# Performance work log

Measured on AMD Instinct MI355X. Metric: run time of the kernel, lower is better.

## Reference

```python
import jax, jax.numpy as jnp
import numpy as np

V, D, L, H, HD, S = 50257, 768, 8, 6, 128, 2048
BS = 128          # flex-attention BLOCK_SIZE
EOS = 50256       # document separator token
EPS = 1.1920929e-07  # torch F.rms_norm default eps (f32 machine eps)
ATTN_SCALE = 0.12


def rms(x):
    return x * jax.lax.rsqrt(jnp.mean(jnp.square(x), axis=-1, keepdims=True) + EPS)


def rope_tables(seq_len, hd):
    # modded-nanogpt rotary: hd//4 geometric freqs + hd//4 zero freqs, applied to half-split dims
    freqs = (1.0 / 1024.0) ** jnp.linspace(0.0, 1.0, hd // 4)
    freqs = jnp.concatenate([freqs, jnp.zeros(hd // 4, dtype=jnp.float32)])
    theta = jnp.arange(seq_len, dtype=jnp.float32)[:, None] * freqs[None, :]  # [S, hd//2]
    return jnp.cos(theta), jnp.sin(theta)


def rope(x, cos, sin):  # x: [B,S,H,hd]
    x1, x2 = jnp.split(x, 2, axis=-1)
    c = cos[None, :, None, :]
    s = sin[None, :, None, :]
    return jnp.concatenate([x1 * c + x2 * s, -x1 * s + x2 * c], axis=-1)


def build_token_mask(input_seq, w):
    # Reproduces BlockMask.from_kv_blocks semantics: per query-row keep the w-1 most
    # recent FULL blocks and min(n_partial, max(w - n_full, 1)) most recent PARTIAL
    # blocks; mask_mod (document-causal) applies inside partial blocks only.
    NB = S // BS
    docs = jnp.cumsum((input_seq == EOS).astype(jnp.int32))
    bi = jnp.arange(NB)
    dr = docs.reshape(NB, BS)
    dl, dh = dr[:, 0], dr[:, -1]
    m_any = (bi[:, None] >= bi[None, :]) & (dl[:, None] <= dh[None, :]) & (dh[:, None] >= dl[None, :])
    m_all = (bi[:, None] > bi[None, :]) & (dl[:, None] == dh[None, :]) & (dh[:, None] == dl[None, :])
    part = m_any & ~m_all
    nf = m_all.sum(-1)

    def keep_most_recent(m, kcount):  # keep kcount True entries with largest kv index
        r = jnp.cumsum(m[:, ::-1].astype(jnp.int32), axis=-1)[:, ::-1]
        return m & (r <= kcount[:, None])

    kf = keep_most_recent(m_all, jnp.minimum(nf, w - 1))
    kp = keep_most_recent(part, jnp.minimum(part.sum(-1), jnp.maximum(w - nf, 1)))
    tf = jnp.repeat(jnp.repeat(kf, BS, 0), BS, 1)   # [S,S]
    tp = jnp.repeat(jnp.repeat(kp, BS, 0), BS, 1)
    q = jnp.arange(S)
    tok = (q[:, None] >= q[None, :]) & (docs[:, None] == docs[None, :])
    return tf | (tp & tok)


def _forward(input_seq, sliding_window_num_blocks, target_seq, embed, ve_embeds,
             qkv_w, attn_proj_w, mlp_fc_w, mlp_proj_w, scalars):
    cos, sin = rope_tables(S, HD)
    long_m = build_token_mask(input_seq, sliding_window_num_blocks)
    short_m = build_token_mask(input_seq, sliding_window_num_blocks // 2)
    cycle = [long_m, short_m, short_m, short_m]
    masks = (cycle * ((L + 3) // 4))[:L - 1] + [long_m]

    ve_tok = ve_embeds[:, input_seq, :]  # [3,S,D]
    ve = [ve_tok[0], ve_tok[1], ve_tok[2]] + [None] * (L - 6) + [ve_tok[0], ve_tok[1], ve_tok[2]]

    skip_w = scalars[:L]
    lambdas = scalars[L:3 * L].reshape(L, 2)
    sa_lambdas = scalars[3 * L:5 * L].reshape(L, 2)

    stride = max(1, L // 4)
    skip_map = {}
    for m in range(3):
        i = L - 3 + m
        j = i - stride * (m + 1)
        if 0 <= j < i < L:
            skip_map[i] = j

    x = x0 = rms(embed[input_seq])[None]  # [1,S,D]
    skips = []
    for i in range(L):
        if i in skip_map:
            x = x + skip_w[skip_map[i]] * skips[skip_map[i]]
        lam, sal = lambdas[i], sa_lambdas[i]
        # Block: residual mix with x0, attn, mlp (modded-nanogpt style)
        x = lam[0] * x + lam[1] * x0
        xa = rms(x)
        qkv = (xa @ qkv_w[i].T).reshape(1, S, 3 * H, HD)
        q, k, v = jnp.split(qkv, 3, axis=2)
        q = rope(rms(q), cos, sin)
        k = rope(rms(k), cos, sin)
        if ve[i] is not None:
            v = sal[0] * v + sal[1] * ve[i].reshape(1, S, H, HD)
        else:
            v = sal[0] * v
        scores = jnp.einsum('bqhd,bkhd->bhqk', q, k) * ATTN_SCALE
        scores = jnp.where(masks[i][None, None], scores, -jnp.inf)
        y = jnp.einsum('bhqk,bkhd->bqhd', jax.nn.softmax(scores, axis=-1), v)
        x = x + y.reshape(1, S, H * HD) @ attn_proj_w[i].T
        h = jnp.square(jax.nn.relu(rms(x) @ mlp_fc_w[i].T))
        x = x + h @ mlp_proj_w[i].T
        skips.append(x)

    x = rms(x)
    logits = (x[0].astype(jnp.bfloat16) @ embed.T.astype(jnp.bfloat16)).astype(jnp.float32)
    cap = 15.0 * logits * jax.lax.rsqrt(jnp.square(logits) + 225.0)  # softcap
    lsm = jax.nn.log_softmax(cap, axis=-1)
    return -jnp.mean(lsm[jnp.arange(S), target_seq])


def setup_inputs() -> dict:
    key = jax.random.key(0)
    ks = jax.random.split(key, 9)
    input_seq = jax.random.randint(ks[0], (S,), 0, V)
    input_seq = input_seq.at[jnp.arange(0, S, 512)].set(EOS)  # inject doc boundaries
    target_seq = jax.random.randint(ks[1], (S,), 0, V)
    embed = jax.random.normal(ks[2], (V, D), jnp.float32)
    ve_embeds = jax.random.normal(ks[3], (3, V, D), jnp.float32)
    sd = 1.0 / np.sqrt(D)
    qkv_w = jax.random.normal(ks[4], (L, 3 * H * HD, D), jnp.float32) * sd
    attn_proj_w = jax.random.normal(ks[5], (L, D, H * HD), jnp.float32) * (1.0 / np.sqrt(H * HD))
    mlp_fc_w = jax.random.normal(ks[6], (L, 4 * D, D), jnp.float32) * sd
    mlp_proj_w = jax.random.normal(ks[7], (L, D, 4 * D), jnp.float32) * (1.0 / np.sqrt(4 * D))
    scalars = jnp.concatenate([
        jnp.ones(L), jnp.tile(jnp.array([1.0, 0.0]), L), jnp.tile(jnp.array([0.5, 0.5]), L)
    ]).astype(jnp.float32) + 0.02 * jax.random.normal(ks[8], (5 * L,), jnp.float32)
    return {"input_seq": input_seq, "sliding_window_num_blocks": 8, "target_seq": target_seq,
            "embed": embed, "ve_embeds": ve_embeds, "qkv_w": qkv_w, "attn_proj_w": attn_proj_w,
            "mlp_fc_w": mlp_fc_w, "mlp_proj_w": mlp_proj_w, "scalars": scalars}


def reference(input_seq, sliding_window_num_blocks, target_seq, embed, ve_embeds,
              qkv_w, attn_proj_w, mlp_fc_w, mlp_proj_w, scalars):
    return _forward(input_seq, sliding_window_num_blocks, target_seq, embed, ve_embeds,
                    qkv_w, attn_proj_w, mlp_fc_w, mlp_proj_w, scalars)
```

## Files before the change

kernel.cpp:

```cpp
#include <hip/hip_runtime.h>
#include <hip/hip_bf16.h>
#include <math.h>

#define NSEQ 2048
#define NDIM 768
#define NLAY 8
#define NHEAD 6
#define NHD 128
#define NVOC 50257
#define NBLK 16
#define BLKSZ 128
#define EOS_TOK 50256
#define EPSF 1.1920929e-07f
#define ASCALE 0.12f
#define NVT 393
#define CAPSH 15.f

#define GSWZ(r) (((r) ^ ((r) >> 2)) & 3)

using bf16x8 = __attribute__((ext_vector_type(8))) __bf16;
using bf16x4 = __attribute__((ext_vector_type(4))) __bf16;
using f32x4  = __attribute__((ext_vector_type(4))) float;

__device__ __forceinline__ __bf16 tobf(float x) {
  __hip_bfloat16 h = __float2bfloat16(x);
  return *reinterpret_cast<__bf16*>(&h);
}

__global__ __launch_bounds__(256) void cvt_bf16_kernel(const float* __restrict__ in, __bf16* __restrict__ out,
                                                       long n) {
  long i = ((long)blockIdx.x * blockDim.x + threadIdx.x) * 4;
  long stride = (long)gridDim.x * blockDim.x * 4;
  for (; i < n; i += stride) {
    float4 v = *(const float4*)(in + i);
    bf16x4 o;
    o[0] = tobf(v.x); o[1] = tobf(v.y); o[2] = tobf(v.z); o[3] = tobf(v.w);
    *(bf16x4*)(out + i) = o;
  }
}

__global__ __launch_bounds__(1024) void prep_kernel(const int* __restrict__ seq, const int* __restrict__ wptr,
                                                    int* __restrict__ docs, int* __restrict__ catL,
                                                    int* __restrict__ catS) {
  __shared__ int f[NSEQ];
  __shared__ int g[NSEQ];
  int tid = threadIdx.x;
  for (int i = tid; i < NSEQ; i += 1024) f[i] = (seq[i] == EOS_TOK) ? 1 : 0;
  __syncthreads();
  int* a = f; int* b = g;
  for (int off = 1; off < NSEQ; off <<= 1) {
    for (int i = tid; i < NSEQ; i += 1024) {
      int v = a[i];
      if (i >= off) v += a[i - off];
      b[i] = v;
    }
    __syncthreads();
    int* t = a; a = b; b = t;
  }
  for (int i = tid; i < NSEQ; i += 1024) docs[i] = a[i];
  __syncthreads();
  if (tid == 0) {
    int dl[NBLK], dh[NBLK];
    for (int bi = 0; bi < NBLK; ++bi) { dl[bi] = a[bi * BLKSZ]; dh[bi] = a[bi * BLKSZ + BLKSZ - 1]; }
    int W = *wptr;
    for (int pass = 0; pass < 2; ++pass) {
      int w = (pass == 0) ? W : (W / 2);
      int* cat = (pass == 0) ? catL : catS;
      for (int i = 0; i < NBLK; ++i) {
        int allr[NBLK], partr[NBLK];
        int nf = 0, np = 0;
        for (int j = 0; j < NBLK; ++j) {
          int any_ = (i >= j) && (dl[i] <= dh[j]) && (dh[i] >= dl[j]);
          int all_ = (i > j) && (dl[i] == dh[j]) && (dh[i] == dl[j]);
          allr[j] = all_; partr[j] = any_ && !all_;
          nf += all_; np += partr[j];
        }
        int kcf = min(nf, w - 1);
        int kcp = min(np, max(w - nf, 1));
        int cf = 0, cp = 0;
        for (int j = NBLK - 1; j >= 0; --j) {
          int cv = 0;
          if (allr[j]) { cf++; if (cf <= kcf) cv = 2; }
          if (partr[j]) { cp++; if (cp <= kcp) cv = 1; }
          cat[i * NBLK + j] = cv;
        }
      }
    }
  }
}

__global__ __launch_bounds__(256) void embed_rms_kernel(const int* __restrict__ seq, const float* __restrict__ embed,
                                                        float* __restrict__ x, float* __restrict__ x0) {
  int s = blockIdx.x;
  int tid = threadIdx.x;
  const float* row = embed + (size_t)seq[s] * NDIM;
  float v0 = row[tid], v1 = row[tid + 256], v2 = row[tid + 512];
  float ss = v0 * v0 + v1 * v1 + v2 * v2;
  __shared__ float red[256];
  red[tid] = ss; __syncthreads();
  for (int o = 128; o > 0; o >>= 1) { if (tid < o) red[tid] += red[tid + o]; __syncthreads(); }
  float sc = rsqrtf(red[0] / (float)NDIM + EPSF);
  size_t base = (size_t)s * NDIM;
  float o0 = v0 * sc, o1 = v1 * sc, o2 = v2 * sc;
  x[base + tid] = o0; x[base + tid + 256] = o1; x[base + tid + 512] = o2;
  x0[base + tid] = o0; x0[base + tid + 256] = o1; x0[base + tid + 512] = o2;
}

__global__ __launch_bounds__(256) void rmsbf_kernel(const float* __restrict__ x, __bf16* __restrict__ xb) {
  int s = blockIdx.x;
  int tid = threadIdx.x;
  size_t base = (size_t)s * NDIM;
  float v0 = x[base + tid], v1 = x[base + tid + 256], v2 = x[base + tid + 512];
  float ss = v0 * v0 + v1 * v1 + v2 * v2;
  __shared__ float red[256];
  red[tid] = ss; __syncthreads();
  for (int o = 128; o > 0; o >>= 1) { if (tid < o) red[tid] += red[tid + o]; __syncthreads(); }
  float sc = rsqrtf(red[0] / (float)NDIM + EPSF);
  xb[base + tid] = tobf(v0 * sc); xb[base + tid + 256] = tobf(v1 * sc); xb[base + tid + 512] = tobf(v2 * sc);
}

__global__ __launch_bounds__(256) void mixrms_kernel(float* __restrict__ x, const float* __restrict__ x0,
                                                     const float* __restrict__ skip, const float* __restrict__ scal,
                                                     int li, int sj, __bf16* __restrict__ xb) {
  float lam0 = scal[NLAY + 2 * li], lam1 = scal[NLAY + 2 * li + 1];
  float sw = (sj >= 0) ? scal[sj] : 0.f;
  int s = blockIdx.x;
  int tid = threadIdx.x;
  size_t base = (size_t)s * NDIM;
  float xv[3], ov[3], nv[3];
  xv[0] = x[base + tid]; xv[1] = x[base + tid + 256]; xv[2] = x[base + tid + 512];
  ov[0] = x0[base + tid]; ov[1] = x0[base + tid + 256]; ov[2] = x0[base + tid + 512];
  if (skip) {
    nv[0] = lam0 * (xv[0] + sw * skip[base + tid])       + lam1 * ov[0];
    nv[1] = lam0 * (xv[1] + sw * skip[base + tid + 256]) + lam1 * ov[1];
    nv[2] = lam0 * (xv[2] + sw * skip[base + tid + 512]) + lam1 * ov[2];
  } else {
    nv[0] = lam0 * xv[0] + lam1 * ov[0];
    nv[1] = lam0 * xv[1] + lam1 * ov[1];
    nv[2] = lam0 * xv[2] + lam1 * ov[2];
  }
  x[base + tid] = nv[0]; x[base + tid + 256] = nv[1]; x[base + tid + 512] = nv[2];
  float ss = nv[0] * nv[0] + nv[1] * nv[1] + nv[2] * nv[2];
  __shared__ float red[256];
  red[tid] = ss; __syncthreads();
  for (int o = 128; o > 0; o >>= 1) { if (tid < o) red[tid] += red[tid + o]; __syncthreads(); }
  float sc = rsqrtf(red[0] / (float)NDIM + EPSF);
  xb[base + tid] = tobf(nv[0] * sc); xb[base + tid + 256] = tobf(nv[1] * sc); xb[base + tid + 512] = tobf(nv[2] * sc);
}

template <int MODE>
__global__ __launch_bounds__(256) void gemm_mfma(const __bf16* __restrict__ A, const __bf16* __restrict__ B,
                                                 float* __restrict__ Cf, __bf16* __restrict__ Cb,
                                                 int N, int K) {
  __shared__ __bf16 As[2][128 * 32];
  __shared__ __bf16 Bs[2][128 * 32];
  int bm = blockIdx.x * 128, bn = blockIdx.y * 128;
  int tid = threadIdx.x;
  int w = tid >> 6, l = tid & 63;
  int wm = (w >> 1) * 64, wn = (w & 1) * 64;
  int c = l & 15, g = l >> 4;

  auto stage = [&](int buf, int k0) {
#pragma unroll
    for (int i = 0; i < 2; ++i) {
      int L = (w * 2 + i) * 64 + l;
      int row = L >> 2, gc = L & 3;
      int gs = gc ^ GSWZ(row);
      const __bf16* srcA = A + (size_t)(bm + row) * K + k0 + gs * 8;
      const __bf16* srcB = B + (size_t)(bn + row) * K + k0 + gs * 8;
      __builtin_amdgcn_global_load_lds(
          (const __attribute__((address_space(1))) void*)srcA,
          (__attribute__((address_space(3))) void*)&As[buf][(w * 2 + i) * 512], 16, 0, 0);
      __builtin_amdgcn_global_load_lds(
          (const __attribute__((address_space(1))) void*)srcB,
          (__attribute__((address_space(3))) void*)&Bs[buf][(w * 2 + i) * 512], 16, 0, 0);
    }
  };

  f32x4 acc[4][4] = {};
  stage(0, 0);
  __syncthreads();
  int nk = K >> 5;
  for (int kk = 0; kk < nk; ++kk) {
    int buf = kk & 1;
    if (kk + 1 < nk) stage(buf ^ 1, (kk + 1) * 32);
    bf16x8 af[4], bfr[4];
#pragma unroll
    for (int i = 0; i < 4; ++i) {
      int row = wm + i * 16 + c;
      af[i] = *(const bf16x8*)&As[buf][row * 32 + (g ^ GSWZ(row)) * 8];
    }
#pragma unroll
    for (int j = 0; j < 4; ++j) {
      int row = wn + j * 16 + c;
      bfr[j] = *(const bf16x8*)&Bs[buf][row * 32 + (g ^ GSWZ(row)) * 8];
    }
#pragma unroll
    for (int i = 0; i < 4; ++i)
#pragma unroll
      for (int j = 0; j < 4; ++j)
        acc[i][j] = __builtin_amdgcn_mfma_f32_16x16x32_bf16(af[i], bfr[j], acc[i][j], 0, 0, 0);
    __syncthreads();
  }
#pragma unroll
  for (int i = 0; i < 4; ++i)
#pragma unroll
    for (int j = 0; j < 4; ++j)
#pragma unroll
      for (int rr = 0; rr < 4; ++rr) {
        int row = bm + wm + i * 16 + g * 4 + rr;
        int col = bn + wn + j * 16 + c;
        size_t ci = (size_t)row * N + col;
        float z = acc[i][j][rr];
        if (MODE == 0) Cf[ci] = z;
        else if (MODE == 1) Cf[ci] += z;
        else { float r = fmaxf(z, 0.f); Cb[ci] = tobf(r * r); }
      }
}

template <int MODE>
__global__ __launch_bounds__(256) void gemm_mfma64(const __bf16* __restrict__ A, const __bf16* __restrict__ B,
                                                   float* __restrict__ Cf, __bf16* __restrict__ Cb,
                                                   int N, int K) {
  __shared__ __bf16 As[2][64 * 32];
  __shared__ __bf16 Bs[2][64 * 32];
  int bm = blockIdx.x * 64, bn = blockIdx.y * 64;
  int tid = threadIdx.x;
  int w = tid >> 6, l = tid & 63;
  int wm = (w >> 1) * 32, wn = (w & 1) * 32;
  int c = l & 15, g = l >> 4;

  auto stage = [&](int buf, int k0) {
    int L = w * 64 + l;
    int row = L >> 2, gc = L & 3;
    int gs = gc ^ GSWZ(row);
    const __bf16* srcA = A + (size_t)(bm + row) * K + k0 + gs * 8;
    const __bf16* srcB = B + (size_t)(bn + row) * K + k0 + gs * 8;
    __builtin_amdgcn_global_load_lds(
        (const __attribute__((address_space(1))) void*)srcA,
        (__attribute__((address_space(3))) void*)&As[buf][w * 512], 16, 0, 0);
    __builtin_amdgcn_global_load_lds(
        (const __attribute__((address_space(1))) void*)srcB,
        (__attribute__((address_space(3))) void*)&Bs[buf][w * 512], 16, 0, 0);
  };

  f32x4 acc[2][2] = {};
  stage(0, 0);
  __syncthreads();
  int nk = K >> 5;
  for (int kk = 0; kk < nk; ++kk) {
    int buf = kk & 1;
    if (kk + 1 < nk) stage(buf ^ 1, (kk + 1) * 32);
    bf16x8 af[2], bfr[2];
#pragma unroll
    for (int i = 0; i < 2; ++i) {
      int row = wm + i * 16 + c;
      af[i] = *(const bf16x8*)&As[buf][row * 32 + (g ^ GSWZ(row)) * 8];
    }
#pragma unroll
    for (int j = 0; j < 2; ++j) {
      int row = wn + j * 16 + c;
      bfr[j] = *(const bf16x8*)&Bs[buf][row * 32 + (g ^ GSWZ(row)) * 8];
    }
#pragma unroll
    for (int i = 0; i < 2; ++i)
#pragma unroll
      for (int j = 0; j < 2; ++j)
        acc[i][j] = __builtin_amdgcn_mfma_f32_16x16x32_bf16(af[i], bfr[j], acc[i][j], 0, 0, 0);
    __syncthreads();
  }
#pragma unroll
  for (int i = 0; i < 2; ++i)
#pragma unroll
    for (int j = 0; j < 2; ++j)
#pragma unroll
      for (int rr = 0; rr < 4; ++rr) {
        int row = bm + wm + i * 16 + g * 4 + rr;
        int col = bn + wn + j * 16 + c;
        size_t ci = (size_t)row * N + col;
        float z = acc[i][j][rr];
        if (MODE == 0) Cf[ci] = z;
        else if (MODE == 1) Cf[ci] += z;
        else { float r = fmaxf(z, 0.f); Cb[ci] = tobf(r * r); }
      }
}

__global__ __launch_bounds__(256) void qkv_post_kernel(const float* __restrict__ qkv, const float* __restrict__ vemb,
                                                       const int* __restrict__ seq, const float* __restrict__ scal,
                                                       int li, int ve_idx,
                                                       __bf16* __restrict__ qo, __bf16* __restrict__ ko,
                                                       __bf16* __restrict__ vo) {
  int p = blockIdx.x * 4 + (threadIdx.x >> 6);
  int l = threadIdx.x & 63;
  int h = p >> 11;
  int s = p & (NSEQ - 1);
  float sal0 = scal[3 * NLAY + 2 * li], sal1 = scal[3 * NLAY + 2 * li + 1];
  float fr = (l < 32) ? powf(1.0f / 1024.0f, (float)l * (1.0f / 31.0f)) : 0.f;
  float th = (float)s * fr;
  float cth = cosf(th), sth = sinf(th);
  size_t rb = (size_t)s * (3 * NHEAD * NHD) + h * NHD;
  float q0 = qkv[rb + l],                 q1 = qkv[rb + l + 64];
  float k0 = qkv[rb + NHEAD * NHD + l],   k1 = qkv[rb + NHEAD * NHD + l + 64];
  float v0 = qkv[rb + 2 * NHEAD * NHD + l], v1 = qkv[rb + 2 * NHEAD * NHD + l + 64];
  float ssq = q0 * q0 + q1 * q1;
  float ssk = k0 * k0 + k1 * k1;
#pragma unroll
  for (int o = 1; o < 64; o <<= 1) {
    ssq += __shfl_xor(ssq, o, 64);
    ssk += __shfl_xor(ssk, o, 64);
  }
  float scq = rsqrtf(ssq / (float)NHD + EPSF);
  float sck = rsqrtf(ssk / (float)NHD + EPSF);
  float qn0 = q0 * scq, qn1 = q1 * scq;
  float kn0 = k0 * sck, kn1 = k1 * sck;
  float oq0 = qn0 * cth + qn1 * sth, oq1 = -qn0 * sth + qn1 * cth;
  float ok0 = kn0 * cth + kn1 * sth, ok1 = -kn0 * sth + kn1 * cth;
  float ov0 = sal0 * v0, ov1 = sal0 * v1;
  if (ve_idx >= 0) {
    const float* ver = vemb + ((size_t)ve_idx * NVOC + seq[s]) * NDIM + h * NHD;
    ov0 += sal1 * ver[l];
    ov1 += sal1 * ver[l + 64];
  }
  size_t oo = ((size_t)h * NSEQ + s) * NHD;
  qo[oo + l] = tobf(oq0); qo[oo + l + 64] = tobf(oq1);
  ko[oo + l] = tobf(ok0); ko[oo + l + 64] = tobf(ok1);
  vo[oo + l] = tobf(ov0); vo[oo + l + 64] = tobf(ov1);
}

__global__ __launch_bounds__(256) void vtrans_kernel(const __bf16* __restrict__ v, __bf16* __restrict__ vt) {
  int st = blockIdx.x * 64, dt = blockIdx.y * 64, h = blockIdx.z;
  __shared__ __bf16 t[64][65];
  int tid = threadIdx.x;
  for (int e = tid; e < 4096; e += 256) {
    int s = e >> 6, d = e & 63;
    t[s][d] = v[((size_t)h * NSEQ + st + s) * NHD + dt + d];
  }
  __syncthreads();
  for (int e = tid; e < 512; e += 256) {
    int d = e >> 3, s0 = (e & 7) * 8;
    bf16x8 ov;
#pragma unroll
    for (int i = 0; i < 8; ++i) ov[i] = t[s0 + i][d];
    *(bf16x8*)(vt + ((size_t)h * NHD + dt + d) * NSEQ + st + s0) = ov;
  }
}

__global__ __launch_bounds__(128) void attn_mfma_kernel(const __bf16* __restrict__ qb, const __bf16* __restrict__ kb,
                                                        const __bf16* __restrict__ vt, const int* __restrict__ cat,
                                                        const int* __restrict__ docs, __bf16* __restrict__ y) {
  int qb32 = (int)gridDim.x - 1 - (int)blockIdx.x;
  int h = blockIdx.y;
  int tid = threadIdx.x;
  int wq = tid >> 6;
  int l = tid & 63;
  int c = l & 15, g = l >> 4;
  int q0 = qb32 * 32 + wq * 16;
  int qB = qb32 >> 2;

  __shared__ __bf16 Ks[2][32 * 128];
  __shared__ __bf16 Vts[2][32 * 128];
  __shared__ __bf16 Ps[2][16 * 32];
  __shared__ int kvs[64];
  __shared__ int kvc[64];
  __shared__ int nact_s;

  if (tid == 0) {
    int n = 0;
    for (int kv = 0; kv <= qb32; ++kv) {
      int cc = cat[qB * NBLK + (kv >> 2)];
      if (cc) { kvs[n] = kv; kvc[n] = cc; ++n; }
    }
    nact_s = n;
  }

  bf16x8 qf[4];
#pragma unroll
  for (int ks = 0; ks < 4; ++ks)
    qf[ks] = *(const bf16x8*)(qb + ((size_t)h * NSEQ + q0 + c) * NHD + ks * 32 + g * 8);

  int qd[4];
#pragma unroll
  for (int rr = 0; rr < 4; ++rr) qd[rr] = docs[q0 + g * 4 + rr];

  float m[4], lden[4];
#pragma unroll
  for (int rr = 0; rr < 4; ++rr) { m[rr] = -INFINITY; lden[rr] = 0.f; }
  f32x4 oacc[8] = {};

  __syncthreads();
  int nact = nact_s;

  auto stage = [&](int kv, int bufi) {
#pragma unroll
    for (int i = 0; i < 4; ++i) {
      int L = (wq * 4 + i) * 64 + l;
      int krow = L >> 4, gl = L & 15;
      int gs = gl ^ (krow & 7);
      const __bf16* srcK = kb + ((size_t)h * NSEQ + kv * 32 + krow) * NHD + gs * 8;
      __builtin_amdgcn_global_load_lds(
          (const __attribute__((address_space(1))) void*)srcK,
          (__attribute__((address_space(3))) void*)&Ks[bufi][(wq * 4 + i) * 512], 16, 0, 0);
      int drow = L >> 2, gk = L & 3;
      const __bf16* srcV = vt + ((size_t)h * NHD + drow) * NSEQ + kv * 32 + gk * 8;
      __builtin_amdgcn_global_load_lds(
          (const __attribute__((address_space(1))) void*)srcV,
          (__attribute__((address_space(3))) void*)&Vts[bufi][(wq * 4 + i) * 512], 16, 0, 0);
    }
  };

  stage(kvs[0], 0);
  __syncthreads();

  for (int it = 0; it < nact; ++it) {
    int buf = it & 1;
    if (it + 1 < nact) stage(kvs[it + 1], buf ^ 1);
    int kv = kvs[it], cc = kvc[it];
    int k0 = kv * 32;

    f32x4 sacc[2] = {};
#pragma unroll
    for (int ks = 0; ks < 4; ++ks) {
#pragma unroll
      for (int j = 0; j < 2; ++j) {
        int row = j * 16 + c;
        int gi = (ks * 4 + g) ^ (row & 7);
        bf16x8 kf = *(const bf16x8*)&Ks[buf][row * 128 + gi * 8];
        sacc[j] = __builtin_amdgcn_mfma_f32_16x16x32_bf16(qf[ks], kf, sacc[j], 0, 0, 0);
      }
    }
    float sc[2][4];
    float bmax[4] = {-INFINITY, -INFINITY, -INFINITY, -INFINITY};
#pragma unroll
    for (int j = 0; j < 2; ++j) {
      int key = k0 + j * 16 + c;
      int kdj = docs[key];
#pragma unroll
      for (int rr = 0; rr < 4; ++rr) {
        int qrow = q0 + g * 4 + rr;
        bool ok = (cc == 2) || ((key <= qrow) && (kdj == qd[rr]));
        float z = ok ? sacc[j][rr] * ASCALE : -INFINITY;
        sc[j][rr] = z;
        bmax[rr] = fmaxf(bmax[rr], z);
      }
    }
#pragma unroll
    for (int rr = 0; rr < 4; ++rr) {
      bmax[rr] = fmaxf(bmax[rr], __shfl_xor(bmax[rr], 1, 64));
      bmax[rr] = fmaxf(bmax[rr], __shfl_xor(bmax[rr], 2, 64));
      bmax[rr] = fmaxf(bmax[rr], __shfl_xor(bmax[rr], 4, 64));
      bmax[rr] = fmaxf(bmax[rr], __shfl_xor(bmax[rr], 8, 64));
    }
    float corr[4], psum[4];
#pragma unroll
    for (int rr = 0; rr < 4; ++rr) {
      float mnew = fmaxf(m[rr], bmax[rr]);
      float msafe = (mnew == -INFINITY) ? 0.f : mnew;
      corr[rr] = __expf(m[rr] - msafe);
      float p0 = __expf(sc[0][rr] - msafe);
      float p1 = __expf(sc[1][rr] - msafe);
      sc[0][rr] = p0; sc[1][rr] = p1;
      psum[rr] = p0 + p1;
      m[rr] = mnew;
    }
#pragma unroll
    for (int rr = 0; rr < 4; ++rr) {
      psum[rr] += __shfl_xor(psum[rr], 1, 64);
      psum[rr] += __shfl_xor(psum[rr], 2, 64);
      psum[rr] += __shfl_xor(psum[rr], 4, 64);
      psum[rr] += __shfl_xor(psum[rr], 8, 64);
      lden[rr] = lden[rr] * corr[rr] + psum[rr];
    }
#pragma unroll
    for (int nt = 0; nt < 8; ++nt)
#pragma unroll
      for (int rr = 0; rr < 4; ++rr) oacc[nt][rr] *= corr[rr];
#pragma unroll
    for (int j = 0; j < 2; ++j)
#pragma unroll
      for (int rr = 0; rr < 4; ++rr)
        Ps[wq][(g * 4 + rr) * 32 + j * 16 + c] = tobf(sc[j][rr]);
    asm volatile("s_waitcnt lgkmcnt(0)" ::: "memory");
    bf16x8 pf = *(const bf16x8*)&Ps[wq][c * 32 + g * 8];
#pragma unroll
    for (int nt = 0; nt < 8; ++nt) {
      bf16x8 vf = *(const bf16x8*)&Vts[buf][(nt * 16 + c) * 32 + g * 8];
      oacc[nt] = __builtin_amdgcn_mfma_f32_16x16x32_bf16(pf, vf, oacc[nt], 0, 0, 0);
    }
    __syncthreads();
  }
  float inv[4];
#pragma unroll
  for (int rr = 0; rr < 4; ++rr) inv[rr] = (lden[rr] > 0.f) ? 1.f / lden[rr] : 0.f;
#pragma unroll
  for (int nt = 0; nt < 8; ++nt)
#pragma unroll
    for (int rr = 0; rr < 4; ++rr) {
      int qrow = q0 + g * 4 + rr;
      y[(size_t)qrow * NDIM + h * NHD + nt * 16 + c] = tobf(oacc[nt][rr] * inv[rr]);
    }
}

__global__ __launch_bounds__(256) void logits_gemm_kernel(const __bf16* __restrict__ xbf,
                                                          const __bf16* __restrict__ embed_bf,
                                                          const int* __restrict__ target,
                                                          float* __restrict__ part_l,
                                                          float* __restrict__ tcap) {
  __shared__ __bf16 As[2][128 * 32];
  __shared__ __bf16 Bs[2][128 * 32];
  __shared__ float rs2[2][128];
  int lid = (int)blockIdx.y * (int)gridDim.x + (int)blockIdx.x;
  int nid = (lid & 7) * 786 + (lid >> 3);
  int bm = (nid & 15) * 128;
  int vt = nid >> 4;
  int bn = vt * 128;
  int tid = threadIdx.x;
  int w = tid >> 6, l = tid & 63;
  int wm = (w >> 1) * 64, wn = (w & 1) * 64;
  int c = l & 15, g = l >> 4;

  auto stage = [&](int buf, int k0) {
#pragma unroll
    for (int i = 0; i < 2; ++i) {
      int L = (w * 2 + i) * 64 + l;
      int row = L >> 2, gc = L & 3;
      int gs = gc ^ GSWZ(row);
      int vrow = bn + row;
      if (vrow >= NVOC) vrow = NVOC - 1;
      const __bf16* srcA = xbf + (size_t)(bm + row) * NDIM + k0 + gs * 8;
      const __bf16* srcB = embed_bf + (size_t)vrow * NDIM + k0 + gs * 8;
      __builtin_amdgcn_global_load_lds(
          (const __attribute__((address_space(1))) void*)srcA,
          (__attribute__((address_space(3))) void*)&As[buf][(w * 2 + i) * 512], 16, 0, 0);
      __builtin_amdgcn_global_load_lds(
          (const __attribute__((address_space(1))) void*)srcB,
          (__attribute__((address_space(3))) void*)&Bs[buf][(w * 2 + i) * 512], 16, 0, 0);
    }
  };

  f32x4 acc[4][4] = {};
  stage(0, 0);
  __syncthreads();
  const int nk = NDIM / 32;
  for (int kk = 0; kk < nk; ++kk) {
    int buf = kk & 1;
    if (kk + 1 < nk) stage(buf ^ 1, (kk + 1) * 32);
    bf16x8 af[4], bfr[4];
#pragma unroll
    for (int i = 0; i < 4; ++i) {
      int row = wm + i * 16 + c;
      af[i] = *(const bf16x8*)&As[buf][row * 32 + (g ^ GSWZ(row)) * 8];
    }
#pragma unroll
    for (int j = 0; j < 4; ++j) {
      int row = wn + j * 16 + c;
      bfr[j] = *(const bf16x8*)&Bs[buf][row * 32 + (g ^ GSWZ(row)) * 8];
    }
#pragma unroll
    for (int i = 0; i < 4; ++i)
#pragma unroll
      for (int j = 0; j < 4; ++j)
        acc[i][j] = __builtin_amdgcn_mfma_f32_16x16x32_bf16(af[i], bfr[j], acc[i][j], 0, 0, 0);
    __syncthreads();
  }

#pragma unroll
  for (int i = 0; i < 4; ++i) {
#pragma unroll
    for (int rr = 0; rr < 4; ++rr) {
      int rowl = wm + i * 16 + g * 4 + rr;
      int tg = target[bm + rowl];
      float ts = 0.f;
#pragma unroll
      for (int j = 0; j < 4; ++j) {
        int vv = bn + wn + j * 16 + c;
        bool okv = vv < NVOC;
        float z = acc[i][j][rr];
        float cp = 15.f * z * rsqrtf(z * z + 225.f);
        ts += okv ? __expf(cp - CAPSH) : 0.f;
        if (okv && vv == tg) tcap[bm + rowl] = cp;
      }
      ts += __shfl_xor(ts, 1, 64);
      ts += __shfl_xor(ts, 2, 64);
      ts += __shfl_xor(ts, 4, 64);
      ts += __shfl_xor(ts, 8, 64);
      if (c == 0) rs2[w & 1][rowl] = ts;
    }
  }
  __syncthreads();
  if (tid < 128) {
    part_l[(size_t)vt * NSEQ + bm + tid] = rs2[0][tid] + rs2[1][tid];
  }
}

__global__ __launch_bounds__(256) void lossrow_kernel(const float* __restrict__ part_l,
                                                      const float* __restrict__ tcap, float* __restrict__ lr) {
  int row = blockIdx.x * 256 + threadIdx.x;
  float L = 0.f;
  for (int cc = 0; cc < NVT; ++cc) L += part_l[(size_t)cc * NSEQ + row];
  lr[row] = (CAPSH + logf(L)) - tcap[row];
}

__global__ __launch_bounds__(256) void loss2_kernel(const float* __restrict__ lr, float* __restrict__ out) {
  int tid = threadIdx.x;
  float sum = 0.f;
  for (int t = tid; t < NSEQ; t += 256) sum += lr[t];
  __shared__ float red[256];
  red[tid] = sum; __syncthreads();
  for (int o = 128; o > 0; o >>= 1) { if (tid < o) red[tid] += red[tid + o]; __syncthreads(); }
  if (tid == 0) out[0] = red[0] / (float)NSEQ;
}

extern "C" void kernel_launch(void* const* d_in, const int* in_sizes, int n_in,
                              void* d_out, int out_size, void* d_ws, size_t ws_size,
                              hipStream_t stream) {
  const int* seq   = (const int*)d_in[0];
  const int* wnb   = (const int*)d_in[1];
  const int* tgt   = (const int*)d_in[2];
  const float* embed = (const float*)d_in[3];
  const float* vemb  = (const float*)d_in[4];
  const float* qkvw  = (const float*)d_in[5];
  const float* aprj  = (const float*)d_in[6];
  const float* fcw   = (const float*)d_in[7];
  const float* prjw  = (const float*)d_in[8];
  const float* scal  = (const float*)d_in[9];
  float* out = (float*)d_out;

  char* w = (char*)d_ws;
  auto alloc = [&](size_t bytes) {
    char* p = w;
    w += (bytes + 255) & ~(size_t)255;
    return p;
  };
  int* docs = (int*)alloc(NSEQ * 4);
  int* catL = (int*)alloc(NBLK * NBLK * 4);
  int* catS = (int*)alloc(NBLK * NBLK * 4);
  float* x    = (float*)alloc((size_t)NSEQ * NDIM * 4);
  float* x0   = (float*)alloc((size_t)NSEQ * NDIM * 4);
  float* sk1  = (float*)alloc((size_t)NSEQ * NDIM * 4);
  float* sk2  = (float*)alloc((size_t)NSEQ * NDIM * 4);
  float* sk3  = (float*)alloc((size_t)NSEQ * NDIM * 4);
  float* qkvb = (float*)alloc((size_t)NSEQ * 3 * NHEAD * NHD * 4);
  __bf16* qbf2 = (__bf16*)alloc((size_t)NHEAD * NSEQ * NHD * 2);
  __bf16* kbf2 = (__bf16*)alloc((size_t)NHEAD * NSEQ * NHD * 2);
  __bf16* vbf2 = (__bf16*)alloc((size_t)NHEAD * NSEQ * NHD * 2);
  __bf16* vtbf = (__bf16*)alloc((size_t)NHEAD * NHD * NSEQ * 2);
  __bf16* xabf = (__bf16*)alloc((size_t)NSEQ * NDIM * 2);
  __bf16* ybf  = (__bf16*)alloc((size_t)NSEQ * NDIM * 2);
  __bf16* hbf  = (__bf16*)alloc((size_t)NSEQ * 4 * NDIM * 2);
  __bf16* xbf  = (__bf16*)alloc((size_t)NSEQ * NDIM * 2);
  float* pl   = (float*)alloc((size_t)NVT * NSEQ * 4);
  float* tc   = (float*)alloc((size_t)NSEQ * 4);
  float* lrow = (float*)alloc((size_t)NSEQ * 4);
  __bf16* embbf = (__bf16*)alloc((size_t)NVOC * NDIM * 2);
  __bf16* qkvwbf = (__bf16*)alloc((size_t)NLAY * 3 * NHEAD * NHD * NDIM * 2);
  __bf16* aprjbf = (__bf16*)alloc((size_t)NLAY * NDIM * NDIM * 2);
  __bf16* fcwbf  = (__bf16*)alloc((size_t)NLAY * 4 * NDIM * NDIM * 2);
  __bf16* prjwbf = (__bf16*)alloc((size_t)NLAY * NDIM * 4 * NDIM * 2);
  float* skips[4] = {nullptr, sk1, sk2, sk3};

  cvt_bf16_kernel<<<2048, 256, 0, stream>>>(embed, embbf, (long)NVOC * NDIM);
  cvt_bf16_kernel<<<2048, 256, 0, stream>>>(qkvw, qkvwbf, (long)NLAY * 3 * NHEAD * NHD * NDIM);
  cvt_bf16_kernel<<<2048, 256, 0, stream>>>(aprj, aprjbf, (long)NLAY * NDIM * NDIM);
  cvt_bf16_kernel<<<2048, 256, 0, stream>>>(fcw, fcwbf, (long)NLAY * 4 * NDIM * NDIM);
  cvt_bf16_kernel<<<2048, 256, 0, stream>>>(prjw, prjwbf, (long)NLAY * NDIM * 4 * NDIM);

  prep_kernel<<<1, 1024, 0, stream>>>(seq, wnb, docs, catL, catS);
  embed_rms_kernel<<<NSEQ, 256, 0, stream>>>(seq, embed, x, x0);

  const int velist[NLAY]   = {0, 1, 2, -1, -1, 0, 1, 2};
  const int skipj[NLAY]    = {-1, -1, -1, -1, -1, 3, 2, 1};
  const int maskLong[NLAY] = {1, 0, 0, 0, 1, 0, 0, 1};

  for (int i = 0; i < NLAY; ++i) {
    mixrms_kernel<<<NSEQ, 256, 0, stream>>>(x, x0, skipj[i] >= 0 ? skips[skipj[i]] : nullptr, scal, i, skipj[i], xabf);
    gemm_mfma64<0><<<dim3(NSEQ / 64, (3 * NHEAD * NHD) / 64), 256, 0, stream>>>(
        xabf, qkvwbf + (size_t)i * 3 * NHEAD * NHD * NDIM, qkvb, nullptr, 3 * NHEAD * NHD, NDIM);
    qkv_post_kernel<<<NHEAD * NSEQ / 4, 256, 0, stream>>>(qkvb, vemb, seq, scal, i, velist[i], qbf2, kbf2, vbf2);
    vtrans_kernel<<<dim3(NSEQ / 64, NHD / 64, NHEAD), 256, 0, stream>>>(vbf2, vtbf);
    attn_mfma_kernel<<<dim3(NSEQ / 32, NHEAD), 128, 0, stream>>>(qbf2, kbf2, vtbf, maskLong[i] ? catL : catS, docs, ybf);
    gemm_mfma64<1><<<dim3(NSEQ / 64, NDIM / 64), 256, 0, stream>>>(
        ybf, aprjbf + (size_t)i * NDIM * NDIM, x, nullptr, NDIM, NDIM);
    rmsbf_kernel<<<NSEQ, 256, 0, stream>>>(x, xabf);
    gemm_mfma64<2><<<dim3(NSEQ / 64, (4 * NDIM) / 64), 256, 0, stream>>>(
        xabf, fcwbf + (size_t)i * 4 * NDIM * NDIM, nullptr, hbf, 4 * NDIM, NDIM);
    gemm_mfma64<1><<<dim3(NSEQ / 64, NDIM / 64), 256, 0, stream>>>(
        hbf, prjwbf + (size_t)i * NDIM * 4 * NDIM, x, nullptr, NDIM, 4 * NDIM);
    if (i >= 1 && i <= 3) {
      hipMemcpyAsync(skips[i], x, (size_t)NSEQ * NDIM * 4, hipMemcpyDeviceToDevice, stream);
    }
  }

  rmsbf_kernel<<<NSEQ, 256, 0, stream>>>(x, xbf);
  logits_gemm_kernel<<<dim3(NSEQ / 128, NVT), 256, 0, stream>>>(xbf, embbf, tgt, pl, tc);
  lossrow_kernel<<<NSEQ / 256, 256, 0, stream>>>(pl, tc, lrow);
  loss2_kernel<<<1, 256, 0, stream>>>(lrow, out);
}
```

Measured before the change: 1.782 ms.

## Split attention KV loop across two wave pairs and merge softmax partials

The attention kernel now launches 256 threads per block. Two pairs of waves each process alternating KV tiles for the same 32 query rows, with separate double-buffered K/V shared-memory regions. At the end the second pair writes its running max, denominator and output accumulators to shared memory, and the first pair merges them flash-decoding style before writing output. This shortens the serial KV chain per block and raises wave-level parallelism. In exchange it uses 64KB of LDS per block, which limits occupancy, and adds a merge step.

```diff
diff --git a/kernel.cpp b/kernel.cpp
--- a/kernel.cpp
+++ b/kernel.cpp
@@ -345,21 +345,24 @@
   }
 }
 
-__global__ __launch_bounds__(128) void attn_mfma_kernel(const __bf16* __restrict__ qb, const __bf16* __restrict__ kb,
+__global__ __launch_bounds__(256) void attn_mfma_kernel(const __bf16* __restrict__ qb, const __bf16* __restrict__ kb,
                                                         const __bf16* __restrict__ vt, const int* __restrict__ cat,
                                                         const int* __restrict__ docs, __bf16* __restrict__ y) {
   int qb32 = (int)gridDim.x - 1 - (int)blockIdx.x;
   int h = blockIdx.y;
   int tid = threadIdx.x;
   int wq = tid >> 6;
+  int pr = wq >> 1;
+  int sub = wq & 1;
   int l = tid & 63;
   int c = l & 15, g = l >> 4;
-  int q0 = qb32 * 32 + wq * 16;
+  int q0 = qb32 * 32 + sub * 16;
   int qB = qb32 >> 2;
 
-  __shared__ __bf16 Ks[2][32 * 128];
-  __shared__ __bf16 Vts[2][32 * 128];
-  __shared__ __bf16 Ps[2][16 * 32];
+  __shared__ __align__(16) char arena[65536];
+  __bf16* Ks  = (__bf16*)arena;
+  __bf16* Vts = (__bf16*)(arena + 32768);
+  __shared__ __bf16 Ps[4][16 * 32];
   __shared__ int kvs[64];
   __shared__ int kvc[64];
   __shared__ int nact_s;
@@ -389,115 +392,148 @@
 
   __syncthreads();
   int nact = nact_s;
-
-  auto stage = [&](int kv, int bufi) {
+  int nit = (nact + 1) >> 1;
+
+  auto stage = [&](int ti, int bufi) {
+    int kv = kvs[ti];
 #pragma unroll
     for (int i = 0; i < 4; ++i) {
-      int L = (wq * 4 + i) * 64 + l;
+      int L = (sub * 4 + i) * 64 + l;
       int krow = L >> 4, gl = L & 15;
       int gs = gl ^ (krow & 7);
       const __bf16* srcK = kb + ((size_t)h * NSEQ + kv * 32 + krow) * NHD + gs * 8;
       __builtin_amdgcn_global_load_lds(
           (const __attribute__((address_space(1))) void*)srcK,
-          (__attribute__((address_space(3))) void*)&Ks[bufi][(wq * 4 + i) * 512], 16, 0, 0);
+          (__attribute__((address_space(3))) void*)&Ks[(pr * 2 + bufi) * 4096 + (sub * 4 + i) * 512], 16, 0, 0);
       int drow = L >> 2, gk = L & 3;
       const __bf16* srcV = vt + ((size_t)h * NHD + drow) * NSEQ + kv * 32 + gk * 8;
       __builtin_amdgcn_global_load_lds(
           (const __attribute__((address_space(1))) void*)srcV,
-          (__attribute__((address_space(3))) void*)&Vts[bufi][(wq * 4 + i) * 512], 16, 0, 0);
+          (__attribute__((address_space(3))) void*)&Vts[(pr * 2 + bufi) * 4096 + (sub * 4 + i) * 512], 16, 0, 0);
     }
   };
 
-  stage(kvs[0], 0);
-  __syncthreads();
-
-  for (int it = 0; it < nact; ++it) {
+  if (pr < nact) stage(pr, 0);
+  __syncthreads();
+
+  for (int it = 0; it < nit; ++it) {
     int buf = it & 1;
-    if (it + 1 < nact) stage(kvs[it + 1], buf ^ 1);
-    int kv = kvs[it], cc = kvc[it];
-    int k0 = kv * 32;
-
-    f32x4 sacc[2] = {};
-#pragma unroll
-    for (int ks = 0; ks < 4; ++ks) {
+    int tin = 2 * (it + 1) + pr;
+    if (tin < nact) stage(tin, buf ^ 1);
+    int ti = 2 * it + pr;
+    if (ti < nact) {
+      int kv = kvs[ti], cc = kvc[ti];
+      int k0 = kv * 32;
+      const __bf16* Kb = &Ks[(pr * 2 + buf) * 4096];
+      const __bf16* Vb = &Vts[(pr * 2 + buf) * 4096];
+
+      f32x4 sacc[2] = {};
+#pragma unroll
+      for (int ks = 0; ks < 4; ++ks) {
+#pragma unroll
+        for (int j = 0; j < 2; ++j) {
+          int row = j * 16 + c;
+          int gi = (ks * 4 + g) ^ (row & 7);
+          bf16x8 kf = *(const bf16x8*)&Kb[row * 128 + gi * 8];
+          sacc[j] = __builtin_amdgcn_mfma_f32_16x16x32_bf16(qf[ks], kf, sacc[j], 0, 0, 0);
+        }
+      }
+      float sc[2][4];
+      float bmax[4] = {-INFINITY, -INFINITY, -INFINITY, -INFINITY};
 #pragma unroll
       for (int j = 0; j < 2; ++j) {
-        int row = j * 16 + c;
-        int gi = (ks * 4 + g) ^ (row & 7);
-        bf16x8 kf = *(const bf16x8*)&Ks[buf][row * 128 + gi * 8];
-        sacc[j] = __builtin_amdgcn_mfma_f32_16x16x32_bf16(qf[ks], kf, sacc[j], 0, 0, 0);
-      }
-    }
-    float sc[2][4];
-    float bmax[4] = {-INFINITY, -INFINITY, -INFINITY, -INFINITY};
-#pragma unroll
-    for (int j = 0; j < 2; ++j) {
-      int key = k0 + j * 16 + c;
-      int kdj = docs[key];
+        int key = k0 + j * 16 + c;
+        int kdj = docs[key];
+#pragma unroll
+        for (int rr = 0; rr < 4; ++rr) {
+          int qrow = q0 + g * 4 + rr;
+          bool ok = (cc == 2) || ((key <= qrow) && (kdj == qd[rr]));
+          float z = ok ? sacc[j][rr] * ASCALE : -INFINITY;
+          sc[j][rr] = z;
+          bmax[rr] = fmaxf(bmax[rr], z);
+        }
+      }
+#pragma unroll
+      for (int rr = 0; rr < 4; ++rr) {
+        bmax[rr] = fmaxf(bmax[rr], __shfl_xor(bmax[rr], 1, 64));
+        bmax[rr] = fmaxf(bmax[rr], __shfl_xor(bmax[rr], 2, 64));
+        bmax[rr] = fmaxf(bmax[rr], __shfl_xor(bmax[rr], 4, 64));
+        bmax[rr] = fmaxf(bmax[rr], __shfl_xor(bmax[rr], 8, 64));
+      }
+      float corr[4], psum[4];
+#pragma unroll
+      for (int rr = 0; rr < 4; ++rr) {
+        float mnew = fmaxf(m[rr], bmax[rr]);
+        float msafe = (mnew == -INFINITY) ? 0.f : mnew;
+        corr[rr] = __expf(m[rr] - msafe);
+        float p0 = __expf(sc[0][rr] - msafe);
+        float p1 = __expf(sc[1][rr] - msafe);
+        sc[0][rr] = p0; sc[1][rr] = p1;
+        psum[rr] = p0 + p1;
+        m[rr] = mnew;
+      }
+#pragma unroll
+      for (int rr = 0; rr < 4; ++rr) {
+        psum[rr] += __shfl_xor(psum[rr], 1, 64);
+        psum[rr] += __shfl_xor(psum[rr], 2, 64);
+        psum[rr] += __shfl_xor(psum[rr], 4, 64);
+        psum[rr] += __shfl_xor(psum[rr], 8, 64);
+        lden[rr] = lden[rr] * corr[rr] + psum[rr];
+      }
+#pragma unroll
+      for (int nt = 0; nt < 8; ++nt)
+#pragma unroll
+        for (int rr = 0; rr < 4; ++rr) oacc[nt][rr] *= corr[rr];
+#pragma unroll
+      for (int j = 0; j < 2; ++j)
+#pragma unroll
+        for (int rr = 0; rr < 4; ++rr)
+          Ps[wq][(g * 4 + rr) * 32 + j * 16 + c] = tobf(sc[j][rr]);
+      asm volatile("s_waitcnt lgkmcnt(0)" ::: "memory");
+      bf16x8 pf = *(const bf16x8*)&Ps[wq][c * 32 + g * 8];
+#pragma unroll
+      for (int nt = 0; nt < 8; ++nt) {
+        bf16x8 vf = *(const bf16x8*)&Vb[(nt * 16 + c) * 32 + g * 8];
+        oacc[nt] = __builtin_amdgcn_mfma_f32_16x16x32_bf16(pf, vf, oacc[nt], 0, 0, 0);
+      }
+    }
+    __syncthreads();
+  }
+
+  float* mrg = (float*)arena;
+  if (pr == 1) {
+    int base = (sub * 64 + l) * 40;
+#pragma unroll
+    for (int rr = 0; rr < 4; ++rr) { mrg[base + rr] = m[rr]; mrg[base + 4 + rr] = lden[rr]; }
+#pragma unroll
+    for (int nt = 0; nt < 8; ++nt)
+#pragma unroll
+      for (int rr = 0; rr < 4; ++rr) mrg[base + 8 + nt * 4 + rr] = oacc[nt][rr];
+  }
+  __syncthreads();
+  if (pr == 0) {
+    int base = (sub * 64 + l) * 40;
+    float w0[4], w1[4], inv[4];
+#pragma unroll
+    for (int rr = 0; rr < 4; ++rr) {
+      float m1v = mrg[base + rr];
+      float l1v = mrg[base + 4 + rr];
+      float M = fmaxf(m[rr], m1v);
+      float msafe = (M == -INFINITY) ? 0.f : M;
+      w0[rr] = __expf(m[rr] - msafe);
+      w1[rr] = __expf(m1v - msafe);
+      float L = lden[rr] * w0[rr] + l1v * w1[rr];
+      inv[rr] = (L > 0.f) ? 1.f / L : 0.f;
+    }
+#pragma unroll
+    for (int nt = 0; nt < 8; ++nt)
 #pragma unroll
       for (int rr = 0; rr < 4; ++rr) {
         int qrow = q0 + g * 4 + rr;
-        bool ok = (cc == 2) || ((key <= qrow) && (kdj == qd[rr]));
-        float z = ok ? sacc[j][rr] * ASCALE : -INFINITY;
-        sc[j][rr] = z;
-        bmax[rr] = fmaxf(bmax[rr], z);
-      }
-    }
-#pragma unroll
-    for (int rr = 0; rr < 4; ++rr) {
-      bmax[rr] = fmaxf(bmax[rr], __shfl_xor(bmax[rr], 1, 64));
-      bmax[rr] = fmaxf(bmax[rr], __shfl_xor(bmax[rr], 2, 64));
-      bmax[rr] = fmaxf(bmax[rr], __shfl_xor(bmax[rr], 4, 64));
-      bmax[rr] = fmaxf(bmax[rr], __shfl_xor(bmax[rr], 8, 64));
-    }
-    float corr[4], psum[4];
-#pragma unroll
-    for (int rr = 0; rr < 4; ++rr) {
-      float mnew = fmaxf(m[rr], bmax[rr]);
-      float msafe = (mnew == -INFINITY) ? 0.f : mnew;
-      corr[rr] = __expf(m[rr] - msafe);
-      float p0 = __expf(sc[0][rr] - msafe);
-      float p1 = __expf(sc[1][rr] - msafe);
-      sc[0][rr] = p0; sc[1][rr] = p1;
-      psum[rr] = p0 + p1;
-      m[rr] = mnew;
-    }
-#pragma unroll
-    for (int rr = 0; rr < 4; ++rr) {
-      psum[rr] += __shfl_xor(psum[rr], 1, 64);
-      psum[rr] += __shfl_xor(psum[rr], 2, 64);
-      psum[rr] += __shfl_xor(psum[rr], 4, 64);
-      psum[rr] += __shfl_xor(psum[rr], 8, 64);
-      lden[rr] = lden[rr] * corr[rr] + psum[rr];
-    }
-#pragma unroll
-    for (int nt = 0; nt < 8; ++nt)
-#pragma unroll
-      for (int rr = 0; rr < 4; ++rr) oacc[nt][rr] *= corr[rr];
-#pragma unroll
-    for (int j = 0; j < 2; ++j)
-#pragma unroll
-      for (int rr = 0; rr < 4; ++rr)
-        Ps[wq][(g * 4 + rr) * 32 + j * 16 + c] = tobf(sc[j][rr]);
-    asm volatile("s_waitcnt lgkmcnt(0)" ::: "memory");
-    bf16x8 pf = *(const bf16x8*)&Ps[wq][c * 32 + g * 8];
-#pragma unroll
-    for (int nt = 0; nt < 8; ++nt) {
-      bf16x8 vf = *(const bf16x8*)&Vts[buf][(nt * 16 + c) * 32 + g * 8];
-      oacc[nt] = __builtin_amdgcn_mfma_f32_16x16x32_bf16(pf, vf, oacc[nt], 0, 0, 0);
-    }
-    __syncthreads();
-  }
-  float inv[4];
-#pragma unroll
-  for (int rr = 0; rr < 4; ++rr) inv[rr] = (lden[rr] > 0.f) ? 1.f / lden[rr] : 0.f;
-#pragma unroll
-  for (int nt = 0; nt < 8; ++nt)
-#pragma unroll
-    for (int rr = 0; rr < 4; ++rr) {
-      int qrow = q0 + g * 4 + rr;
-      y[(size_t)qrow * NDIM + h * NHD + nt * 16 + c] = tobf(oacc[nt][rr] * inv[rr]);
-    }
+        float o = oacc[nt][rr] * w0[rr] + mrg[base + 8 + nt * 4 + rr] * w1[rr];
+        y[(size_t)qrow * NDIM + h * NHD + nt * 16 + c] = tobf(o * inv[rr]);
+      }
+  }
 }
 
 __global__ __launch_bounds__(256) void logits_gemm_kernel(const __bf16* __restrict__ xbf,
@@ -677,7 +713,7 @@
         xabf, qkvwbf + (size_t)i * 3 * NHEAD * NHD * NDIM, qkvb, nullptr, 3 * NHEAD * NHD, NDIM);
     qkv_post_kernel<<<NHEAD * NSEQ / 4, 256, 0, stream>>>(qkvb, vemb, seq, scal, i, velist[i], qbf2, kbf2, vbf2);
     vtrans_kernel<<<dim3(NSEQ / 64, NHD / 64, NHEAD), 256, 0, stream>>>(vbf2, vtbf);
-    attn_mfma_kernel<<<dim3(NSEQ / 32, NHEAD), 128, 0, stream>>>(qbf2, kbf2, vtbf, maskLong[i] ? catL : catS, docs, ybf);
+    attn_mfma_kernel<<<dim3(NSEQ / 32, NHEAD), 256, 0, stream>>>(qbf2, kbf2, vtbf, maskLong[i] ? catL : catS, docs, ybf);
     gemm_mfma64<1><<<dim3(NSEQ / 64, NDIM / 64), 256, 0, stream>>>(
         ybf, aprjbf + (size_t)i * NDIM * NDIM, x, nullptr, NDIM, NDIM);
     rmsbf_kernel<<<NSEQ, 256, 0, stream>>>(x, xabf);
```

Result: faster. 1.694 ms (-5.0%).
